# Optimization experiments

Hardware: AMD Instinct MI355X
Metric: run time of the kernel (lower is better)

## Reference

```python
import jax, jax.numpy as jnp
import numpy as np

N = 8192
F_IN = 128
D = 128
NEG_SLOPE = 0.2  # cfg.negativeslope (standard GAT value)
MASK_FILL = -9e15


def setup_inputs() -> dict:
    key = jax.random.key(0)
    k1, k2, k3, k4 = jax.random.split(key, 4)
    A = jax.random.randint(k1, (N, N), 0, 2, dtype=jnp.int32)
    X = jax.random.normal(k2, (N, F_IN), dtype=jnp.float32)
    # glorot init for Ws, xavier_uniform(gain=1.414) for a
    lim_w = float(np.sqrt(6.0 / (F_IN + D)))
    Ws = jax.random.uniform(k3, (F_IN, D), minval=-lim_w, maxval=lim_w, dtype=jnp.float32)
    lim_a = 1.414 * float(np.sqrt(6.0 / (2 * D + 1)))
    a = jax.random.uniform(k4, (2 * D, 1), minval=-lim_a, maxval=lim_a, dtype=jnp.float32)
    return {"A": A, "X": X, "Ws": Ws, "a": a}


def reference(A, X, Ws, a):
    # Wh: [N, D]
    Wh = X @ Ws
    d = Wh.shape[-1]
    # additive attention: e_ij = leaky_relu(Wh_i . a1 + Wh_j . a2)
    e1 = Wh @ a[:d]          # [N, 1]
    e2 = Wh @ a[d:]          # [N, 1]
    e = jax.nn.leaky_relu(e1 + e2.T, negative_slope=NEG_SLOPE)  # [N, N]
    e = jnp.where(A > 0, e, MASK_FILL)
    attn = jax.nn.softmax(e, axis=1)  # row-wise over neighbors
    H = attn @ Wh            # [N, D]
    return H
```

## Files before the change

kernel.cpp:

```cpp
#include <hip/hip_runtime.h>
#include <hip/hip_bf16.h>

#define NN 8192
#define DD 128

typedef __attribute__((ext_vector_type(8))) short short8;
typedef __attribute__((ext_vector_type(4))) float f32x4;
typedef unsigned int u32;

__device__ __forceinline__ ushort f2bf(float f) {
    __hip_bfloat16 h = __float2bfloat16(f);
    return *(ushort*)&h;
}

__device__ __forceinline__ void async_ld16(const void* g, void* l) {
    __builtin_amdgcn_global_load_lds(
        (const __attribute__((address_space(1))) u32*)g,
        (__attribute__((address_space(3))) u32*)l, 16, 0, 0);
}

__global__ __launch_bounds__(256) void k1_gemm(const float* __restrict__ X,
                                               const float* __restrict__ Ws,
                                               float* __restrict__ Wh) {
    __shared__ float lWs[128 * 132];
    __shared__ float lX[32 * 132];
    int t = threadIdx.x, bx = blockIdx.x;
    const float4* Ws4 = (const float4*)Ws;
    const float4* X4 = (const float4*)X;
    for (int j = 0; j < 16; ++j) {
        int u = j * 256 + t;
        int k = u >> 5, c4 = u & 31;
        *(float4*)&lWs[k * 132 + c4 * 4] = Ws4[u];
    }
    for (int j = 0; j < 4; ++j) {
        int u = j * 256 + t;
        int r = u >> 5, c4 = u & 31;
        *(float4*)&lX[r * 132 + c4 * 4] = X4[bx * 1024 + u];
    }
    __syncthreads();
    int r0 = (t >> 5) * 4, c0 = (t & 31) * 4;
    float acc[4][4];
#pragma unroll
    for (int i = 0; i < 4; ++i)
#pragma unroll
        for (int j = 0; j < 4; ++j) acc[i][j] = 0.f;
#pragma unroll 4
    for (int k = 0; k < 128; ++k) {
        float4 wv = *(const float4*)&lWs[k * 132 + c0];
        float x0 = lX[(r0 + 0) * 132 + k];
        float x1 = lX[(r0 + 1) * 132 + k];
        float x2 = lX[(r0 + 2) * 132 + k];
        float x3 = lX[(r0 + 3) * 132 + k];
#pragma unroll
        for (int j = 0; j < 4; ++j) {
            acc[0][j] += x0 * ((const float*)&wv)[j];
            acc[1][j] += x1 * ((const float*)&wv)[j];
            acc[2][j] += x2 * ((const float*)&wv)[j];
            acc[3][j] += x3 * ((const float*)&wv)[j];
        }
    }
#pragma unroll
    for (int i = 0; i < 4; ++i)
        *(float4*)&Wh[(size_t)(bx * 32 + r0 + i) * 128 + c0] =
            (float4){acc[i][0], acc[i][1], acc[i][2], acc[i][3]};
}

__global__ __launch_bounds__(256) void k2_prep(const float* __restrict__ Wh,
                                               const float* __restrict__ a,
                                               ushort* __restrict__ WhT,
                                               float* __restrict__ C1,
                                               float* __restrict__ C1s,
                                               float* __restrict__ E2p,
                                               float* __restrict__ E2n) {
    __shared__ float lT[128 * 65];
    __shared__ float la[256];
    int t = threadIdx.x;
    int i0 = blockIdx.x * 64;
    la[t] = a[t];
    for (int j = 0; j < 32; ++j) {
        int u = j * 256 + t;
        int r = u >> 7, c = u & 127;
        lT[c * 65 + r] = Wh[(size_t)(i0 + r) * 128 + c];
    }
    __syncthreads();
    int r = t >> 2, q = t & 3;
    float s1 = 0.f, s2 = 0.f;
    for (int j = 0; j < 32; ++j) {
        int d = q * 32 + j;
        float v = lT[d * 65 + r];
        s1 += v * la[d];
        s2 += v * la[128 + d];
    }
    s1 += __shfl_xor(s1, 1); s1 += __shfl_xor(s1, 2);
    s2 += __shfl_xor(s2, 1); s2 += __shfl_xor(s2, 2);
    if (q == 0) {
        int i = i0 + r;
        C1[i]  = __expf(s1);
        C1s[i] = __expf(0.2f * s1);
        E2p[i] = __expf(s2);
        E2n[i] = __expf(0.2f * s2);
    }
    int d = t >> 1, hf = t & 1;
    __attribute__((aligned(16))) ushort tmp[32];
#pragma unroll
    for (int s = 0; s < 32; ++s) tmp[s] = f2bf(lT[d * 65 + hf * 32 + s]);
    uint4* dst = (uint4*)&WhT[(size_t)d * NN + i0 + hf * 32];
    const uint4* srcv = (const uint4*)tmp;
#pragma unroll
    for (int s = 0; s < 4; ++s) dst[s] = srcv[s];
}

__global__ __launch_bounds__(1024, 4) void k3_main(
    const int* __restrict__ A, const ushort* __restrict__ WhT,
    const float* __restrict__ C1, const float* __restrict__ C1s,
    const float* __restrict__ E2p, const float* __restrict__ E2n,
    float* __restrict__ Hp, float* __restrict__ Lp) {

    __shared__ __align__(16) char lB[2 * 32768];
    __shared__ __align__(16) char lA[2 * 32768];

    int tid = threadIdx.x;
    int lane = tid & 63;
    int wv = tid >> 6;
    int g = wv & 3;
    int h = wv >> 2;
    int n = lane & 15;
    int kg = lane >> 4;

    int bx = blockIdx.x;
    int kb = blockIdx.y;
    int row = bx * 64 + g * 16 + n;

    float c1 = C1[row], c1s = C1s[row];

    int p0 = wv * 2;
    int tp0 = p0 >> 3, cp0 = p0 & 7;
    int tp1 = (p0 + 1) >> 3, cp1 = (p0 + 1) & 7;
    int ga0 = p0 >> 3, ta0 = (p0 >> 1) & 3, qa0 = p0 & 1;
    int ga1 = (p0 + 1) >> 3, ta1 = ((p0 + 1) >> 1) & 3, qa1 = (p0 + 1) & 1;

    const ushort* srcB0 = WhT + (size_t)(cp0 * 16 + n) * NN + tp0 * 32 + kg * 8;
    const ushort* srcB1 = WhT + (size_t)(cp1 * 16 + n) * NN + tp1 * 32 + kg * 8;
    const int* srcA0 = A + (size_t)(bx * 64 + ga0 * 16 + n) * NN + ta0 * 32 + kg * 8 + qa0 * 4;
    const int* srcA1 = A + (size_t)(bx * 64 + ga1 * 16 + n) * NN + ta1 * 32 + kg * 8 + qa1 * 4;
    char* dstB0 = lB + p0 * 1024 + lane * 16;
    char* dstB1 = lB + (p0 + 1) * 1024 + lane * 16;
    char* dstA0 = lA + p0 * 1024 + lane * 16;
    char* dstA1 = lA + (p0 + 1) * 1024 + lane * 16;

    const size_t kbase = (size_t)kb * 2048;

    short8 ones;
#pragma unroll
    for (int j = 0; j < 8; ++j) ones[j] = (short)0x3F80;

    f32x4 acc0 = (f32x4){0.f, 0.f, 0.f, 0.f};
    f32x4 acc1 = (f32x4){0.f, 0.f, 0.f, 0.f};
    f32x4 accl = (f32x4){0.f, 0.f, 0.f, 0.f};

    {
        size_t k0 = kbase;
        async_ld16(srcB0 + k0, dstB0);
        async_ld16(srcB1 + k0, dstB1);
        async_ld16(srcA0 + k0, dstA0);
        async_ld16(srcA1 + k0, dstA1);
    }
    __syncthreads();

    for (int kt = 0; kt < 16; ++kt) {
        int b = kt & 1;
        if (kt < 15) {
            size_t kn = kbase + (kt + 1) * 128;
            int bo = (b ^ 1) * 32768;
            async_ld16(srcB0 + kn, dstB0 + bo);
            async_ld16(srcB1 + kn, dstB1 + bo);
            async_ld16(srcA0 + kn, dstA0 + bo);
            async_ld16(srcA1 + kn, dstA1 + bo);
        }
        const char* bufA = lA + b * 32768;
        const char* bufB = lB + b * 32768;
#pragma unroll
        for (int tp = 0; tp < 4; ++tp) {
            const int4* areg = (const int4*)(bufA + (g * 8 + tp * 2) * 1024);
            int4 a0 = areg[lane];
            int4 a1 = areg[64 + lane];
            int kgl = (int)kbase + kt * 128 + tp * 32 + kg * 8;
            float4 pa = *(const float4*)(E2p + kgl);
            float4 pb = *(const float4*)(E2p + kgl + 4);
            float4 na = *(const float4*)(E2n + kgl);
            float4 nb = *(const float4*)(E2n + kgl + 4);
            int am[8]; float ep[8], en[8];
            *(int4*)(am) = a0;     *(int4*)(am + 4) = a1;
            *(float4*)(ep) = pa;   *(float4*)(ep + 4) = pb;
            *(float4*)(en) = na;   *(float4*)(en + 4) = nb;
            short8 af;
#pragma unroll
            for (int u = 0; u < 8; ++u) {
                float w = fmaxf(c1 * ep[u], c1s * en[u]);
                w = am[u] ? w : 0.f;
                af[u] = (short)f2bf(w);
            }
            const short8* bb = (const short8*)(bufB + tp * 8192);
            acc0 = __builtin_amdgcn_mfma_f32_16x16x32_bf16(af, bb[(2 * h + 0) * 64 + lane], acc0, 0, 0, 0);
            acc1 = __builtin_amdgcn_mfma_f32_16x16x32_bf16(af, bb[(2 * h + 1) * 64 + lane], acc1, 0, 0, 0);
            accl = __builtin_amdgcn_mfma_f32_16x16x32_bf16(af, ones, accl, 0, 0, 0);
        }
        __syncthreads();
    }

    if (h == 0 && n == 0) {
#pragma unroll
        for (int r = 0; r < 4; ++r)
            Lp[(size_t)kb * NN + bx * 64 + g * 16 + kg * 4 + r] = accl[r];
    }
    float* Hpb = Hp + (size_t)kb * (NN * DD);
#pragma unroll
    for (int r = 0; r < 4; ++r) {
        int orow = bx * 64 + g * 16 + kg * 4 + r;
        Hpb[(size_t)orow * DD + h * 32 + n] = acc0[r];
        Hpb[(size_t)orow * DD + h * 32 + 16 + n] = acc1[r];
    }
}

__global__ void k4_final(const float* __restrict__ Hp, const float* __restrict__ Lp,
                         float* __restrict__ out) {
    int idx = blockIdx.x * 256 + threadIdx.x;
    int i = idx >> 7;
    float sv = Hp[idx] + Hp[1048576 + idx] + Hp[2097152 + idx] + Hp[3145728 + idx];
    float l = Lp[i] + Lp[8192 + i] + Lp[16384 + i] + Lp[24576 + i];
    out[idx] = sv / l;
}

extern "C" void kernel_launch(void* const* d_in, const int* in_sizes, int n_in,
                              void* d_out, int out_size, void* d_ws, size_t ws_size,
                              hipStream_t stream) {
    const int*   A  = (const int*)d_in[0];
    const float* X  = (const float*)d_in[1];
    const float* Ws = (const float*)d_in[2];
    const float* a  = (const float*)d_in[3];
    float* out = (float*)d_out;

    char* ws = (char*)d_ws;
    float*  Wh  = (float*)(ws);
    ushort* WhT = (ushort*)(ws + (4u << 20));
    float*  C1  = (float*)(ws + (6u << 20));
    float*  C1s = (float*)(ws + (6u << 20) + (32u << 10));
    float*  E2p = (float*)(ws + (6u << 20) + (96u << 10));
    float*  E2n = (float*)(ws + (6u << 20) + (128u << 10));
    float*  Hp  = (float*)(ws + (8u << 20));
    float*  Lp  = (float*)(ws + (24u << 20));

    k1_gemm<<<256, 256, 0, stream>>>(X, Ws, Wh);
    k2_prep<<<128, 256, 0, stream>>>(Wh, a, WhT, C1, C1s, E2p, E2n);
    k3_main<<<dim3(128, 4), 1024, 0, stream>>>(A, WhT, C1, C1s, E2p, E2n, Hp, Lp);
    k4_final<<<4096, 256, 0, stream>>>(Hp, Lp, out);
}
```

Baseline: 461.5 us.

## Pre-pack adjacency into bitmasks and widen per-wave output tile with atomic reduction

A new pre-pass packs the int32 adjacency matrix into 32-bit bitmasks and zeroes the accumulators. The main kernel then reads these small masks in place of streaming A through LDS. Each wave now covers all 128 output columns, so every attention weight it computes feeds 8 MFMAs instead of 2, which cuts the repeated exp/max VALU work. The E2 exponent pairs are interleaved and staged through LDS, and partial sums are combined with atomicAdd rather than written as split-K partial buffers. The cost is an extra full pass over A, float atomic contention, and non-deterministic summation order.

```diff
diff --git a/kernel.cpp b/kernel.cpp
--- a/kernel.cpp
+++ b/kernel.cpp
@@ -70,8 +70,7 @@
                                                ushort* __restrict__ WhT,
                                                float* __restrict__ C1,
                                                float* __restrict__ C1s,
-                                               float* __restrict__ E2p,
-                                               float* __restrict__ E2n) {
+                                               float2* __restrict__ E2) {
     __shared__ float lT[128 * 65];
     __shared__ float la[256];
     int t = threadIdx.x;
@@ -97,8 +96,7 @@
         int i = i0 + r;
         C1[i]  = __expf(s1);
         C1s[i] = __expf(0.2f * s1);
-        E2p[i] = __expf(s2);
-        E2n[i] = __expf(0.2f * s2);
+        E2[i]  = make_float2(__expf(s2), __expf(0.2f * s2));
     }
     int d = t >> 1, hf = t & 1;
     __attribute__((aligned(16))) ushort tmp[32];
@@ -110,125 +108,144 @@
     for (int s = 0; s < 4; ++s) dst[s] = srcv[s];
 }
 
-__global__ __launch_bounds__(1024, 4) void k3_main(
-    const int* __restrict__ A, const ushort* __restrict__ WhT,
+__global__ __launch_bounds__(256) void k0_pack(const int* __restrict__ A,
+                                               u32* __restrict__ Ap,
+                                               float* __restrict__ Hp,
+                                               float* __restrict__ Lp) {
+    u32 u = blockIdx.x * 256 + threadIdx.x;
+    if (u < (u32)(NN * DD)) Hp[u] = 0.f;
+    if (u < (u32)NN) Lp[u] = 0.f;
+    u32 kt = u >> 15;
+    u32 row = (u >> 2) & (NN - 1);
+    u32 kg = u & 3;
+    const int* base = A + (size_t)row * NN + kt * 128 + kg * 8;
+    u32 d = 0;
+#pragma unroll
+    for (int tp = 0; tp < 4; ++tp) {
+        int4 lo = *(const int4*)(base + tp * 32);
+        int4 hi = *(const int4*)(base + tp * 32 + 4);
+        u32 b = 0;
+        b |= (lo.x != 0) ? 1u : 0u;
+        b |= (lo.y != 0) ? 2u : 0u;
+        b |= (lo.z != 0) ? 4u : 0u;
+        b |= (lo.w != 0) ? 8u : 0u;
+        b |= (hi.x != 0) ? 16u : 0u;
+        b |= (hi.y != 0) ? 32u : 0u;
+        b |= (hi.z != 0) ? 64u : 0u;
+        b |= (hi.w != 0) ? 128u : 0u;
+        d |= b << (8 * tp);
+    }
+    Ap[u] = d;
+}
+
+__global__ __launch_bounds__(512, 4) void k3_main(
+    const u32* __restrict__ Ap, const ushort* __restrict__ WhT,
     const float* __restrict__ C1, const float* __restrict__ C1s,
-    const float* __restrict__ E2p, const float* __restrict__ E2n,
+    const float2* __restrict__ E2,
     float* __restrict__ Hp, float* __restrict__ Lp) {
 
     __shared__ __align__(16) char lB[2 * 32768];
-    __shared__ __align__(16) char lA[2 * 32768];
+    __shared__ __align__(16) char lE[2 * 1024];
 
     int tid = threadIdx.x;
     int lane = tid & 63;
-    int wv = tid >> 6;
-    int g = wv & 3;
-    int h = wv >> 2;
+    int w = tid >> 6;
     int n = lane & 15;
     int kg = lane >> 4;
 
     int bx = blockIdx.x;
     int kb = blockIdx.y;
-    int row = bx * 64 + g * 16 + n;
+    int rb = bx * 128 + w * 16;
+    int row = rb + n;
+    int kt0 = kb * 8;
 
     float c1 = C1[row], c1s = C1s[row];
 
-    int p0 = wv * 2;
-    int tp0 = p0 >> 3, cp0 = p0 & 7;
-    int tp1 = (p0 + 1) >> 3, cp1 = (p0 + 1) & 7;
-    int ga0 = p0 >> 3, ta0 = (p0 >> 1) & 3, qa0 = p0 & 1;
-    int ga1 = (p0 + 1) >> 3, ta1 = ((p0 + 1) >> 1) & 3, qa1 = (p0 + 1) & 1;
-
-    const ushort* srcB0 = WhT + (size_t)(cp0 * 16 + n) * NN + tp0 * 32 + kg * 8;
-    const ushort* srcB1 = WhT + (size_t)(cp1 * 16 + n) * NN + tp1 * 32 + kg * 8;
-    const int* srcA0 = A + (size_t)(bx * 64 + ga0 * 16 + n) * NN + ta0 * 32 + kg * 8 + qa0 * 4;
-    const int* srcA1 = A + (size_t)(bx * 64 + ga1 * 16 + n) * NN + ta1 * 32 + kg * 8 + qa1 * 4;
-    char* dstB0 = lB + p0 * 1024 + lane * 16;
-    char* dstB1 = lB + (p0 + 1) * 1024 + lane * 16;
-    char* dstA0 = lA + p0 * 1024 + lane * 16;
-    char* dstA1 = lA + (p0 + 1) * 1024 + lane * 16;
-
-    const size_t kbase = (size_t)kb * 2048;
+    const char* srcB[4];
+    char* dstB[4];
+#pragma unroll
+    for (int i = 0; i < 4; ++i) {
+        int p = 4 * w + i;
+        int c = p & 7, tp = p >> 3;
+        srcB[i] = (const char*)(WhT + (size_t)(c * 16 + n) * NN +
+                                (size_t)kt0 * 128 + tp * 32 + kg * 8);
+        dstB[i] = lB + p * 1024 + lane * 16;
+    }
+    const char* srcE = (const char*)(E2 + (size_t)kt0 * 128) + lane * 16;
+
+    const u32* pA = Ap + ((size_t)kt0 * NN + row) * 4 + kg;
+    u32 a_cur = pA[0];
+    u32 a_nxt = 0;
+
+#pragma unroll
+    for (int i = 0; i < 4; ++i) async_ld16(srcB[i], dstB[i]);
+    if (w == 0) async_ld16(srcE, lE + lane * 16);
 
     short8 ones;
 #pragma unroll
     for (int j = 0; j < 8; ++j) ones[j] = (short)0x3F80;
 
-    f32x4 acc0 = (f32x4){0.f, 0.f, 0.f, 0.f};
-    f32x4 acc1 = (f32x4){0.f, 0.f, 0.f, 0.f};
+    f32x4 acc[8];
+#pragma unroll
+    for (int c = 0; c < 8; ++c) acc[c] = (f32x4){0.f, 0.f, 0.f, 0.f};
     f32x4 accl = (f32x4){0.f, 0.f, 0.f, 0.f};
 
-    {
-        size_t k0 = kbase;
-        async_ld16(srcB0 + k0, dstB0);
-        async_ld16(srcB1 + k0, dstB1);
-        async_ld16(srcA0 + k0, dstA0);
-        async_ld16(srcA1 + k0, dstA1);
-    }
     __syncthreads();
 
-    for (int kt = 0; kt < 16; ++kt) {
-        int b = kt & 1;
-        if (kt < 15) {
-            size_t kn = kbase + (kt + 1) * 128;
-            int bo = (b ^ 1) * 32768;
-            async_ld16(srcB0 + kn, dstB0 + bo);
-            async_ld16(srcB1 + kn, dstB1 + bo);
-            async_ld16(srcA0 + kn, dstA0 + bo);
-            async_ld16(srcA1 + kn, dstA1 + bo);
+    for (int kt = 0; kt < 8; ++kt) {
+        int buf = kt & 1;
+        if (kt < 7) {
+            int bo = (buf ^ 1) * 32768;
+#pragma unroll
+            for (int i = 0; i < 4; ++i)
+                async_ld16(srcB[i] + (kt + 1) * 256, dstB[i] + bo);
+            if (w == 0)
+                async_ld16(srcE + (kt + 1) * 1024, lE + (buf ^ 1) * 1024 + lane * 16);
+            a_nxt = pA[(size_t)(kt + 1) * (NN * 4)];
         }
-        const char* bufA = lA + b * 32768;
-        const char* bufB = lB + b * 32768;
+        const char* bB = lB + buf * 32768;
+        const float* bE = (const float*)(lE + buf * 1024);
 #pragma unroll
         for (int tp = 0; tp < 4; ++tp) {
-            const int4* areg = (const int4*)(bufA + (g * 8 + tp * 2) * 1024);
-            int4 a0 = areg[lane];
-            int4 a1 = areg[64 + lane];
-            int kgl = (int)kbase + kt * 128 + tp * 32 + kg * 8;
-            float4 pa = *(const float4*)(E2p + kgl);
-            float4 pb = *(const float4*)(E2p + kgl + 4);
-            float4 na = *(const float4*)(E2n + kgl);
-            float4 nb = *(const float4*)(E2n + kgl + 4);
-            int am[8]; float ep[8], en[8];
-            *(int4*)(am) = a0;     *(int4*)(am + 4) = a1;
-            *(float4*)(ep) = pa;   *(float4*)(ep + 4) = pb;
-            *(float4*)(en) = na;   *(float4*)(en + 4) = nb;
+            const float4* ev = (const float4*)(bE + (tp * 32 + kg * 8) * 2);
+            float pe[16];
+            *(float4*)(pe + 0)  = ev[0];
+            *(float4*)(pe + 4)  = ev[1];
+            *(float4*)(pe + 8)  = ev[2];
+            *(float4*)(pe + 12) = ev[3];
+            u32 ab = (a_cur >> (tp * 8)) & 0xffu;
             short8 af;
 #pragma unroll
             for (int u = 0; u < 8; ++u) {
-                float w = fmaxf(c1 * ep[u], c1s * en[u]);
-                w = am[u] ? w : 0.f;
-                af[u] = (short)f2bf(w);
+                float wv = fmaxf(c1 * pe[2 * u], c1s * pe[2 * u + 1]);
+                af[u] = ((ab >> u) & 1u) ? (short)f2bf(wv) : (short)0;
             }
-            const short8* bb = (const short8*)(bufB + tp * 8192);
-            acc0 = __builtin_amdgcn_mfma_f32_16x16x32_bf16(af, bb[(2 * h + 0) * 64 + lane], acc0, 0, 0, 0);
-            acc1 = __builtin_amdgcn_mfma_f32_16x16x32_bf16(af, bb[(2 * h + 1) * 64 + lane], acc1, 0, 0, 0);
+            const short8* bb = (const short8*)(bB + tp * 8192);
+#pragma unroll
+            for (int c = 0; c < 8; ++c)
+                acc[c] = __builtin_amdgcn_mfma_f32_16x16x32_bf16(
+                    af, bb[c * 64 + lane], acc[c], 0, 0, 0);
             accl = __builtin_amdgcn_mfma_f32_16x16x32_bf16(af, ones, accl, 0, 0, 0);
         }
+        a_cur = a_nxt;
         __syncthreads();
     }
 
-    if (h == 0 && n == 0) {
+#pragma unroll
+    for (int c = 0; c < 8; ++c)
 #pragma unroll
         for (int r = 0; r < 4; ++r)
-            Lp[(size_t)kb * NN + bx * 64 + g * 16 + kg * 4 + r] = accl[r];
-    }
-    float* Hpb = Hp + (size_t)kb * (NN * DD);
-#pragma unroll
-    for (int r = 0; r < 4; ++r) {
-        int orow = bx * 64 + g * 16 + kg * 4 + r;
-        Hpb[(size_t)orow * DD + h * 32 + n] = acc0[r];
-        Hpb[(size_t)orow * DD + h * 32 + 16 + n] = acc1[r];
-    }
+            atomicAdd(&Hp[(size_t)(rb + kg * 4 + r) * DD + c * 16 + n], acc[c][r]);
+    if (n == 0)
+#pragma unroll
+        for (int r = 0; r < 4; ++r)
+            atomicAdd(&Lp[rb + kg * 4 + r], accl[r]);
 }
 
 __global__ void k4_final(const float* __restrict__ Hp, const float* __restrict__ Lp,
                          float* __restrict__ out) {
     int idx = blockIdx.x * 256 + threadIdx.x;
-    int i = idx >> 7;
-    float sv = Hp[idx] + Hp[1048576 + idx] + Hp[2097152 + idx] + Hp[3145728 + idx];
-    float l = Lp[i] + Lp[8192 + i] + Lp[16384 + i] + Lp[24576 + i];
-    out[idx] = sv / l;
+    out[idx] = Hp[idx] / Lp[idx >> 7];
 }
 
 extern "C" void kernel_launch(void* const* d_in, const int* in_sizes, int n_in,
@@ -241,17 +258,18 @@
     float* out = (float*)d_out;
 
     char* ws = (char*)d_ws;
+    u32*    Ap  = (u32*)(ws);
     float*  Wh  = (float*)(ws);
-    ushort* WhT = (ushort*)(ws + (4u << 20));
-    float*  C1  = (float*)(ws + (6u << 20));
-    float*  C1s = (float*)(ws + (6u << 20) + (32u << 10));
-    float*  E2p = (float*)(ws + (6u << 20) + (96u << 10));
-    float*  E2n = (float*)(ws + (6u << 20) + (128u << 10));
-    float*  Hp  = (float*)(ws + (8u << 20));
-    float*  Lp  = (float*)(ws + (24u << 20));
+    ushort* WhT = (ushort*)(ws + (8u << 20));
+    float*  C1  = (float*)(ws + (10u << 20));
+    float*  C1s = (float*)(ws + (10u << 20) + (32u << 10));
+    float2* E2  = (float2*)(ws + (10u << 20) + (64u << 10));
+    float*  Hp  = (float*)(ws + (10u << 20) + (128u << 10));
+    float*  Lp  = (float*)(ws + (14u << 20) + (128u << 10));
 
     k1_gemm<<<256, 256, 0, stream>>>(X, Ws, Wh);
-    k2_prep<<<128, 256, 0, stream>>>(Wh, a, WhT, C1, C1s, E2p, E2n);
-    k3_main<<<dim3(128, 4), 1024, 0, stream>>>(A, WhT, C1, C1s, E2p, E2n, Hp, Lp);
+    k2_prep<<<128, 256, 0, stream>>>(Wh, a, WhT, C1, C1s, E2);
+    k0_pack<<<8192, 256, 0, stream>>>(A, Ap, Hp, Lp);
+    k3_main<<<dim3(64, 8), 512, 0, stream>>>(Ap, WhT, C1, C1s, E2, Hp, Lp);
     k4_final<<<4096, 256, 0, stream>>>(Hp, Lp, out);
 }
```

After: 451.2 us. -2.2%, faster.
